# Kernel optimization log

Hardware: AMD Instinct MI355X
Metric: run time of the kernel (lower is better)

The kernel has to match this reference:

```python
import jax, jax.numpy as jnp
import numpy as np

B, L, C, H = 2, 512, 256, 8
D = C // H
LN_EPS = 1e-5


def setup_inputs() -> dict:
    key = jax.random.key(0)
    ks = jax.random.split(key, 9)
    s = lambda fan: 1.0 / np.sqrt(fan)
    return {
        "x": jax.random.normal(ks[0], (B, L, C), dtype=jnp.float32),
        "relative_pos": jax.random.normal(ks[1], (B, L, L, C), dtype=jnp.float32),
        "w_qkv": jax.random.normal(ks[2], (3 * C, C), dtype=jnp.float32) * s(C),
        "w_rel": jax.random.normal(ks[3], (H, C), dtype=jnp.float32) * s(C),
        "b_rel": jax.random.normal(ks[4], (H,), dtype=jnp.float32) * 0.02,
        "ln_gamma": jnp.ones((H,), dtype=jnp.float32),
        "ln_beta": jnp.zeros((H,), dtype=jnp.float32),
        "w_proj": jax.random.normal(ks[5], (C, C), dtype=jnp.float32) * s(C),
        "b_proj": jnp.zeros((C,), dtype=jnp.float32),
    }


def reference(x, relative_pos, w_qkv, w_rel, b_rel, ln_gamma, ln_beta, w_proj, b_proj):
    scale = D ** -0.5
    # qkv projection: [B,L,3C] -> [3,B,H,L,D]
    qkv = (x @ w_qkv.T).reshape(B, L, 3, H, D).transpose(2, 0, 3, 1, 4)
    q, k, v = qkv[0], qkv[1], qkv[2]
    # relative bias: Linear -> exact GELU -> LayerNorm over head dim
    rel = relative_pos @ w_rel.T + b_rel          # [B,L,L,H]
    rel = jax.nn.gelu(rel, approximate=False)
    mu = jnp.mean(rel, axis=-1, keepdims=True)
    var = jnp.mean(jnp.square(rel - mu), axis=-1, keepdims=True)
    rel = (rel - mu) * jax.lax.rsqrt(var + LN_EPS) * ln_gamma + ln_beta
    rel = rel.transpose(0, 3, 1, 2)               # [B,H,L,L]
    # attention (bias added pre-scale, matching the original)
    attn = (jnp.einsum("bhld,bhmd->bhlm", q, k) + rel) * scale
    attn = jax.nn.softmax(attn, axis=-1)
    out = jnp.einsum("bhlm,bhmd->bhld", attn, v)  # [B,H,L,D]
    out = out.transpose(0, 2, 1, 3).reshape(B, L, C)
    return out @ w_proj.T + b_proj
```

## Files before the change

### kernel.cpp

```cpp
#include <hip/hip_runtime.h>
#include <hip/hip_bf16.h>
#include <math.h>

#define BB 2
#define LL 512
#define CC 256
#define HH 8
#define DD 32
#define LN_EPS 1e-5f
#define SCALE 0.17677669529663687f

__global__ __launch_bounds__(256) void k1_qkv(const float* __restrict__ x,
                                              const float* __restrict__ w,
                                              float* __restrict__ qkv_out) {
    __shared__ float xs[16][64];
    __shared__ float wsd[16][64];
    const int row0 = blockIdx.x * 64;
    const int col0 = blockIdx.y * 64;
    const int t  = threadIdx.x;
    const int ry = t >> 4;
    const int cx = t & 15;
    const int lr = t >> 2;
    const int lq = t & 3;
    float acc[4][4] = {};
    for (int k0 = 0; k0 < 256; k0 += 16) {
        float4 xv = *(const float4*)(x + (row0 + lr) * 256 + k0 + 4 * lq);
        float4 wv = *(const float4*)(w + (col0 + lr) * 256 + k0 + 4 * lq);
        xs[4*lq+0][lr] = xv.x; xs[4*lq+1][lr] = xv.y;
        xs[4*lq+2][lr] = xv.z; xs[4*lq+3][lr] = xv.w;
        wsd[4*lq+0][lr] = wv.x; wsd[4*lq+1][lr] = wv.y;
        wsd[4*lq+2][lr] = wv.z; wsd[4*lq+3][lr] = wv.w;
        __syncthreads();
#pragma unroll
        for (int kk = 0; kk < 16; ++kk) {
            float4 a  = *(const float4*)&xs[kk][4*ry];
            float4 bb = *(const float4*)&wsd[kk][4*cx];
            float av[4] = {a.x, a.y, a.z, a.w};
            float bv[4] = {bb.x, bb.y, bb.z, bb.w};
#pragma unroll
            for (int rr = 0; rr < 4; ++rr)
#pragma unroll
                for (int cc = 0; cc < 4; ++cc)
                    acc[rr][cc] = fmaf(av[rr], bv[cc], acc[rr][cc]);
        }
        __syncthreads();
    }
#pragma unroll
    for (int rr = 0; rr < 4; ++rr) {
        const int row = row0 + 4*ry + rr;
        const int b = row >> 9, l = row & 511;
#pragma unroll
        for (int cc = 0; cc < 4; ++cc) {
            const int o = col0 + 4*cx + cc;
            const int three = o >> 8;
            const int hh = (o >> 5) & 7;
            const int dd = o & 31;
            qkv_out[three * 262144 + ((b*8 + hh)*512 + l)*32 + dd] = acc[rr][cc];
        }
    }
}

__global__ __launch_bounds__(256) void k2_rel(const float* __restrict__ rp,
                                              const float* __restrict__ wr,
                                              const float* __restrict__ br,
                                              const float* __restrict__ gam_p,
                                              const float* __restrict__ bet_p,
                                              float* __restrict__ rel) {
    const int lane = threadIdx.x & 63;
    const int wid  = blockIdx.x * 4 + (threadIdx.x >> 6);
    float4 wv[8];
#pragma unroll
    for (int h = 0; h < 8; ++h)
        wv[h] = *(const float4*)(wr + h * 256 + 4 * lane);
    const int s = lane >> 3;
    const float bre = br[s];
    const float gam = gam_p[s];
    const float bet = bet_p[s];

    for (int it = 0; it < 128; ++it) {
        const long pos = (long)wid + (long)it * 4096;
        float4 a = *(const float4*)(rp + pos * 256 + 4 * lane);
        float p[8];
#pragma unroll
        for (int h = 0; h < 8; ++h) {
            float acc = a.x * wv[h].x;
            acc = fmaf(a.y, wv[h].y, acc);
            acc = fmaf(a.z, wv[h].z, acc);
            acc = fmaf(a.w, wv[h].w, acc);
            p[h] = acc;
        }
#pragma unroll
        for (int h = 0; h < 8; ++h) {
            p[h] += __shfl_xor(p[h], 8);
            p[h] += __shfl_xor(p[h], 16);
            p[h] += __shfl_xor(p[h], 32);
        }
        float a0 = (s & 1) ? p[1] : p[0];
        float a1 = (s & 1) ? p[3] : p[2];
        float a2 = (s & 1) ? p[5] : p[4];
        float a3 = (s & 1) ? p[7] : p[6];
        float b0 = (s & 2) ? a1 : a0;
        float b1 = (s & 2) ? a3 : a2;
        float rv = (s & 4) ? b1 : b0;
        rv += __shfl_xor(rv, 1);
        rv += __shfl_xor(rv, 2);
        rv += __shfl_xor(rv, 4);
        rv += bre;
        float g = 0.5f * rv * (1.0f + erff(rv * 0.70710678118654752f));
        float sg = g, sg2 = g * g;
        sg  += __shfl_xor(sg, 8);   sg2 += __shfl_xor(sg2, 8);
        sg  += __shfl_xor(sg, 16);  sg2 += __shfl_xor(sg2, 16);
        sg  += __shfl_xor(sg, 32);  sg2 += __shfl_xor(sg2, 32);
        const float mu  = sg * 0.125f;
        const float var = fmaf(sg2, 0.125f, -mu * mu);
        const float o = fmaf((g - mu) * rsqrtf(var + LN_EPS), gam, bet);
        const float ov = __shfl(o, (lane & 7) * 8);
        if (lane < 8) rel[pos * 8 + lane] = ov;
    }
}

__global__ __launch_bounds__(256) void k3_attn(const float* __restrict__ qg,
                                               const float* __restrict__ kg,
                                               const float* __restrict__ vg,
                                               const float* __restrict__ rel,
                                               float* __restrict__ outg) {
    __shared__ float p_lds[4][512];
    const int lane = threadIdx.x & 63;
    const int wid  = threadIdx.x >> 6;
    const int row  = blockIdx.x * 4 + wid;
    const int b = row >> 12;
    const int h = (row >> 9) & 7;
    const int i = row & 511;

    const float* qp = qg + ((b*8 + h)*512 + i) * 32;
    float4 qv[8];
#pragma unroll
    for (int dd = 0; dd < 8; ++dd)
        qv[dd] = *(const float4*)(qp + 4 * dd);

    const float* kp0  = kg + (long)((b*8 + h)*512) * 32;
    const float* relp = rel + ((long)(b*512 + i) * 512) * 8 + h;

    float sc[8];
#pragma unroll
    for (int t = 0; t < 8; ++t) {
        const int j = lane + 64 * t;
        const float* kp = kp0 + j * 32;
        float acc = 0.0f;
#pragma unroll
        for (int dd = 0; dd < 8; ++dd) {
            float4 k4 = *(const float4*)(kp + 4 * dd);
            acc = fmaf(qv[dd].x, k4.x, acc);
            acc = fmaf(qv[dd].y, k4.y, acc);
            acc = fmaf(qv[dd].z, k4.z, acc);
            acc = fmaf(qv[dd].w, k4.w, acc);
        }
        const float rl = relp[(long)j * 8];
        sc[t] = (acc + rl) * SCALE;
    }
    float m = sc[0];
#pragma unroll
    for (int t = 1; t < 8; ++t) m = fmaxf(m, sc[t]);
    m = fmaxf(m, __shfl_xor(m, 1));
    m = fmaxf(m, __shfl_xor(m, 2));
    m = fmaxf(m, __shfl_xor(m, 4));
    m = fmaxf(m, __shfl_xor(m, 8));
    m = fmaxf(m, __shfl_xor(m, 16));
    m = fmaxf(m, __shfl_xor(m, 32));
    float sum = 0.0f;
#pragma unroll
    for (int t = 0; t < 8; ++t) { sc[t] = __expf(sc[t] - m); sum += sc[t]; }
    sum += __shfl_xor(sum, 1);
    sum += __shfl_xor(sum, 2);
    sum += __shfl_xor(sum, 4);
    sum += __shfl_xor(sum, 8);
    sum += __shfl_xor(sum, 16);
    sum += __shfl_xor(sum, 32);
    const float inv = 1.0f / sum;
#pragma unroll
    for (int t = 0; t < 8; ++t)
        p_lds[wid][lane + 64 * t] = sc[t] * inv;
    __syncthreads();

    const int d = lane & 31;
    const int half = lane >> 5;
    const float* vp = vg + (long)((b*8 + h)*512) * 32 + d;
    const float* pw = &p_lds[wid][half * 256];
    float acc = 0.0f;
#pragma unroll 4
    for (int jj = 0; jj < 256; ++jj)
        acc = fmaf(pw[jj], vp[(half * 256 + jj) * 32], acc);
    acc += __shfl_xor(acc, 32);
    if (lane < 32)
        outg[(b*512 + i) * 256 + h * 32 + d] = acc;
}

__global__ __launch_bounds__(256) void k4_proj(const float* __restrict__ a_in,
                                               const float* __restrict__ w,
                                               const float* __restrict__ bp,
                                               float* __restrict__ outg) {
    __shared__ float xs[16][64];
    __shared__ float wsd[16][64];
    const int row0 = blockIdx.x * 64;
    const int col0 = blockIdx.y * 64;
    const int t  = threadIdx.x;
    const int ry = t >> 4;
    const int cx = t & 15;
    const int lr = t >> 2;
    const int lq = t & 3;
    float acc[4][4] = {};
    for (int k0 = 0; k0 < 256; k0 += 16) {
        float4 xv = *(const float4*)(a_in + (row0 + lr) * 256 + k0 + 4 * lq);
        float4 wv = *(const float4*)(w + (col0 + lr) * 256 + k0 + 4 * lq);
        xs[4*lq+0][lr] = xv.x; xs[4*lq+1][lr] = xv.y;
        xs[4*lq+2][lr] = xv.z; xs[4*lq+3][lr] = xv.w;
        wsd[4*lq+0][lr] = wv.x; wsd[4*lq+1][lr] = wv.y;
        wsd[4*lq+2][lr] = wv.z; wsd[4*lq+3][lr] = wv.w;
        __syncthreads();
#pragma unroll
        for (int kk = 0; kk < 16; ++kk) {
            float4 a  = *(const float4*)&xs[kk][4*ry];
            float4 bb = *(const float4*)&wsd[kk][4*cx];
            float av[4] = {a.x, a.y, a.z, a.w};
            float bv[4] = {bb.x, bb.y, bb.z, bb.w};
#pragma unroll
            for (int rr = 0; rr < 4; ++rr)
#pragma unroll
                for (int cc = 0; cc < 4; ++cc)
                    acc[rr][cc] = fmaf(av[rr], bv[cc], acc[rr][cc]);
        }
        __syncthreads();
    }
#pragma unroll
    for (int rr = 0; rr < 4; ++rr) {
        const int row = row0 + 4*ry + rr;
#pragma unroll
        for (int cc = 0; cc < 4; ++cc) {
            const int col = col0 + 4*cx + cc;
            outg[row * 256 + col] = acc[rr][cc] + bp[col];
        }
    }
}

extern "C" void kernel_launch(void* const* d_in, const int* in_sizes, int n_in,
                              void* d_out, int out_size, void* d_ws, size_t ws_size,
                              hipStream_t stream) {
    const float* x      = (const float*)d_in[0];
    const float* rp     = (const float*)d_in[1];
    const float* w_qkv  = (const float*)d_in[2];
    const float* w_rel  = (const float*)d_in[3];
    const float* b_rel  = (const float*)d_in[4];
    const float* gamma  = (const float*)d_in[5];
    const float* beta   = (const float*)d_in[6];
    const float* w_proj = (const float*)d_in[7];
    const float* b_proj = (const float*)d_in[8];
    float* out = (float*)d_out;
    float* ws  = (float*)d_ws;

    float* q    = ws;
    float* kk   = ws + 262144;
    float* vv   = ws + 524288;
    float* rel  = ws + 786432;
    float* attn = ws + 786432 + 4194304;

    k1_qkv<<<dim3(16, 12), 256, 0, stream>>>(x, w_qkv, q);
    k2_rel<<<1024, 256, 0, stream>>>(rp, w_rel, b_rel, gamma, beta, rel);
    k3_attn<<<2048, 256, 0, stream>>>(q, kk, vv, rel, attn);
    k4_proj<<<dim3(16, 4), 256, 0, stream>>>(attn, w_proj, b_proj, out);
}
```

Baseline: 912.1 us.

## Restructure relative-bias kernel with LDS tiling and transposed bias layout

New measurement: 826.9 us. 9.3% less time.

```diff
diff --git a/kernel.cpp b/kernel.cpp
--- a/kernel.cpp
+++ b/kernel.cpp
@@ -9,6 +9,7 @@
 #define DD 32
 #define LN_EPS 1e-5f
 #define SCALE 0.17677669529663687f
+#define RSQRT2 0.70710678118654752f
 
 __global__ __launch_bounds__(256) void k1_qkv(const float* __restrict__ x,
                                               const float* __restrict__ w,
@@ -65,64 +66,66 @@
                                               const float* __restrict__ br,
                                               const float* __restrict__ gam_p,
                                               const float* __restrict__ bet_p,
-                                              float* __restrict__ rel) {
-    const int lane = threadIdx.x & 63;
-    const int wid  = blockIdx.x * 4 + (threadIdx.x >> 6);
-    float4 wv[8];
-#pragma unroll
-    for (int h = 0; h < 8; ++h)
-        wv[h] = *(const float4*)(wr + h * 256 + 4 * lane);
-    const int s = lane >> 3;
-    const float bre = br[s];
-    const float gam = gam_p[s];
-    const float bet = bet_p[s];
-
-    for (int it = 0; it < 128; ++it) {
-        const long pos = (long)wid + (long)it * 4096;
-        float4 a = *(const float4*)(rp + pos * 256 + 4 * lane);
-        float p[8];
-#pragma unroll
-        for (int h = 0; h < 8; ++h) {
-            float acc = a.x * wv[h].x;
-            acc = fmaf(a.y, wv[h].y, acc);
-            acc = fmaf(a.z, wv[h].z, acc);
-            acc = fmaf(a.w, wv[h].w, acc);
-            p[h] = acc;
-        }
-#pragma unroll
-        for (int h = 0; h < 8; ++h) {
-            p[h] += __shfl_xor(p[h], 8);
-            p[h] += __shfl_xor(p[h], 16);
-            p[h] += __shfl_xor(p[h], 32);
-        }
-        float a0 = (s & 1) ? p[1] : p[0];
-        float a1 = (s & 1) ? p[3] : p[2];
-        float a2 = (s & 1) ? p[5] : p[4];
-        float a3 = (s & 1) ? p[7] : p[6];
-        float b0 = (s & 2) ? a1 : a0;
-        float b1 = (s & 2) ? a3 : a2;
-        float rv = (s & 4) ? b1 : b0;
-        rv += __shfl_xor(rv, 1);
-        rv += __shfl_xor(rv, 2);
-        rv += __shfl_xor(rv, 4);
-        rv += bre;
-        float g = 0.5f * rv * (1.0f + erff(rv * 0.70710678118654752f));
-        float sg = g, sg2 = g * g;
-        sg  += __shfl_xor(sg, 8);   sg2 += __shfl_xor(sg2, 8);
-        sg  += __shfl_xor(sg, 16);  sg2 += __shfl_xor(sg2, 16);
-        sg  += __shfl_xor(sg, 32);  sg2 += __shfl_xor(sg2, 32);
-        const float mu  = sg * 0.125f;
-        const float var = fmaf(sg2, 0.125f, -mu * mu);
-        const float o = fmaf((g - mu) * rsqrtf(var + LN_EPS), gam, bet);
-        const float ov = __shfl(o, (lane & 7) * 8);
-        if (lane < 8) rel[pos * 8 + lane] = ov;
-    }
+                                              float* __restrict__ rel_t) {
+    __shared__ float rps[32 * 260];
+    __shared__ float wls[8 * 260];
+    __shared__ float st[8][33];
+    const int t   = threadIdx.x;
+    const int blk = blockIdx.x;
+    const int jt  = blk & 15;
+    const int i   = (blk >> 4) & 511;
+    const int b   = blk >> 13;
+    const int j0  = jt << 5;
+
+    {
+        const float4* ws4 = (const float4*)wr;
+        int idx = t;
+        int hh = idx >> 6, c4 = idx & 63;
+        *(float4*)&wls[hh * 260 + 4 * c4] = ws4[idx];
+        idx = t + 256;
+        hh = idx >> 6; c4 = idx & 63;
+        *(float4*)&wls[hh * 260 + 4 * c4] = ws4[idx];
+    }
+    const int jr = t >> 3;
+    const int u  = t & 7;
+    const float4* rsrc = (const float4*)(rp + (((long)(b * 512 + i) * 512) + j0 + jr) * 256);
+#pragma unroll
+    for (int c = 0; c < 8; ++c)
+        *(float4*)&rps[jr * 260 + 4 * (u + 8 * c)] = rsrc[u + 8 * c];
+    __syncthreads();
+
+    const int h = t & 7;
+    const float* ar   = &rps[jr * 260];
+    const float* wrow = &wls[h * 260];
+    float4 acc = {0.f, 0.f, 0.f, 0.f};
+#pragma unroll 8
+    for (int c4 = 0; c4 < 64; ++c4) {
+        float4 a = *(const float4*)&ar[4 * c4];
+        float4 w = *(const float4*)&wrow[4 * c4];
+        acc.x = fmaf(a.x, w.x, acc.x);
+        acc.y = fmaf(a.y, w.y, acc.y);
+        acc.z = fmaf(a.z, w.z, acc.z);
+        acc.w = fmaf(a.w, w.w, acc.w);
+    }
+    float r = ((acc.x + acc.y) + (acc.z + acc.w)) + br[h];
+    float g = 0.5f * r * (1.0f + erff(r * RSQRT2));
+    float sg = g, sg2 = g * g;
+    sg += __shfl_xor(sg, 1); sg2 += __shfl_xor(sg2, 1);
+    sg += __shfl_xor(sg, 2); sg2 += __shfl_xor(sg2, 2);
+    sg += __shfl_xor(sg, 4); sg2 += __shfl_xor(sg2, 4);
+    const float mu  = sg * 0.125f;
+    const float var = fmaf(sg2, 0.125f, -mu * mu);
+    const float o = fmaf((g - mu) * rsqrtf(var + LN_EPS), gam_p[h], bet_p[h]);
+    st[h][jr] = o;
+    __syncthreads();
+    const int h2 = t >> 5, j2 = t & 31;
+    rel_t[(((long)(b * 8 + h2) * 512) + i) * 512 + j0 + j2] = st[h2][j2];
 }
 
 __global__ __launch_bounds__(256) void k3_attn(const float* __restrict__ qg,
                                                const float* __restrict__ kg,
                                                const float* __restrict__ vg,
-                                               const float* __restrict__ rel,
+                                               const float* __restrict__ rel_t,
                                                float* __restrict__ outg) {
     __shared__ float p_lds[4][512];
     const int lane = threadIdx.x & 63;
@@ -139,12 +142,12 @@
         qv[dd] = *(const float4*)(qp + 4 * dd);
 
     const float* kp0  = kg + (long)((b*8 + h)*512) * 32;
-    const float* relp = rel + ((long)(b*512 + i) * 512) * 8 + h;
+    const float* relp = rel_t + (((long)(b*8 + h)*512) + i) * 512;
 
     float sc[8];
 #pragma unroll
-    for (int t = 0; t < 8; ++t) {
-        const int j = lane + 64 * t;
+    for (int tt = 0; tt < 8; ++tt) {
+        const int j = lane + 64 * tt;
         const float* kp = kp0 + j * 32;
         float acc = 0.0f;
 #pragma unroll
@@ -155,12 +158,11 @@
             acc = fmaf(qv[dd].z, k4.z, acc);
             acc = fmaf(qv[dd].w, k4.w, acc);
         }
-        const float rl = relp[(long)j * 8];
-        sc[t] = (acc + rl) * SCALE;
+        sc[tt] = (acc + relp[j]) * SCALE;
     }
     float m = sc[0];
 #pragma unroll
-    for (int t = 1; t < 8; ++t) m = fmaxf(m, sc[t]);
+    for (int tt = 1; tt < 8; ++tt) m = fmaxf(m, sc[tt]);
     m = fmaxf(m, __shfl_xor(m, 1));
     m = fmaxf(m, __shfl_xor(m, 2));
     m = fmaxf(m, __shfl_xor(m, 4));
@@ -169,7 +171,7 @@
     m = fmaxf(m, __shfl_xor(m, 32));
     float sum = 0.0f;
 #pragma unroll
-    for (int t = 0; t < 8; ++t) { sc[t] = __expf(sc[t] - m); sum += sc[t]; }
+    for (int tt = 0; tt < 8; ++tt) { sc[tt] = __expf(sc[tt] - m); sum += sc[tt]; }
     sum += __shfl_xor(sum, 1);
     sum += __shfl_xor(sum, 2);
     sum += __shfl_xor(sum, 4);
@@ -178,18 +180,23 @@
     sum += __shfl_xor(sum, 32);
     const float inv = 1.0f / sum;
 #pragma unroll
-    for (int t = 0; t < 8; ++t)
-        p_lds[wid][lane + 64 * t] = sc[t] * inv;
+    for (int tt = 0; tt < 8; ++tt)
+        p_lds[wid][lane + 64 * tt] = sc[tt] * inv;
     __syncthreads();
 
     const int d = lane & 31;
     const int half = lane >> 5;
-    const float* vp = vg + (long)((b*8 + h)*512) * 32 + d;
+    const float* vp = vg + (long)((b*8 + h)*512) * 32 + (half * 256) * 32 + d;
     const float* pw = &p_lds[wid][half * 256];
-    float acc = 0.0f;
+    float a0 = 0.f, a1 = 0.f, a2 = 0.f, a3 = 0.f;
 #pragma unroll 4
-    for (int jj = 0; jj < 256; ++jj)
-        acc = fmaf(pw[jj], vp[(half * 256 + jj) * 32], acc);
+    for (int jj = 0; jj < 256; jj += 4) {
+        a0 = fmaf(pw[jj + 0], vp[(jj + 0) * 32], a0);
+        a1 = fmaf(pw[jj + 1], vp[(jj + 1) * 32], a1);
+        a2 = fmaf(pw[jj + 2], vp[(jj + 2) * 32], a2);
+        a3 = fmaf(pw[jj + 3], vp[(jj + 3) * 32], a3);
+    }
+    float acc = (a0 + a1) + (a2 + a3);
     acc += __shfl_xor(acc, 32);
     if (lane < 32)
         outg[(b*512 + i) * 256 + h * 32 + d] = acc;
@@ -257,14 +264,14 @@
     float* out = (float*)d_out;
     float* ws  = (float*)d_ws;
 
-    float* q    = ws;
-    float* kk   = ws + 262144;
-    float* vv   = ws + 524288;
-    float* rel  = ws + 786432;
-    float* attn = ws + 786432 + 4194304;
+    float* q     = ws;
+    float* kk    = ws + 262144;
+    float* vv    = ws + 524288;
+    float* rel_t = ws + 786432;
+    float* attn  = ws + 786432 + 4194304;
 
     k1_qkv<<<dim3(16, 12), 256, 0, stream>>>(x, w_qkv, q);
-    k2_rel<<<1024, 256, 0, stream>>>(rp, w_rel, b_rel, gamma, beta, rel);
-    k3_attn<<<2048, 256, 0, stream>>>(q, kk, vv, rel, attn);
+    k2_rel<<<16384, 256, 0, stream>>>(rp, w_rel, b_rel, gamma, beta, rel_t);
+    k3_attn<<<2048, 256, 0, stream>>>(q, kk, vv, rel_t, attn);
     k4_proj<<<dim3(16, 4), 256, 0, stream>>>(attn, w_proj, b_proj, out);
 }
```
